# Optimization experiments

Hardware: AMD Instinct MI355X
Metric: run time of the kernel (lower is better)

The kernel has to match this reference:

```python
import jax, jax.numpy as jnp
from jax import lax
import numpy as np

B, C, T, S = 128, 512, 512, 128
L = 2 * S + 1  # blank-extended label length


def _ext_labels(seq, blank):
    # Channel index for each extended-label position s: blank at even s, seq[(s-1)//2] at odd s.
    s = jnp.arange(L)
    l = jnp.maximum(0, (s - 1) // 2)
    return jnp.where(s % 2 == 0, blank, seq[l])


def _alpha_pass(probs, lab):
    # probs: [C, T] per-frame probabilities; lab: [L] extended label channel ids.
    # Faithful to compute_alpha(): per-frame renormalization (Rabiner scaling) and
    # start-window masking (s >= L - 2*(T - t)); entries beyond end = 2t+2 are
    # structurally exact zeros, so summing the full masked column equals the
    # original's windowed sum.
    s = jnp.arange(L)
    p_ext = probs[lab, :].T  # [T, L]
    lab_m2 = jnp.concatenate([jnp.full((2,), -1, lab.dtype), lab[:-2]])
    # s-2 transition allowed only at odd s with non-repeated label (s==1 handled by zero pad).
    mask2 = (s % 2 == 1) & (lab != lab_m2)

    a0 = jnp.zeros(L, probs.dtype).at[0].set(p_ext[0, 0]).at[1].set(p_ext[0, 1])
    c0 = a0.sum()
    a0 = jnp.where(c0 > 0, a0 / c0, a0)

    def step(a_prev, inp):
        t, p_t = inp
        start = jnp.maximum(0, L - 2 * (T - t))
        a1 = jnp.concatenate([jnp.zeros(1, a_prev.dtype), a_prev[:-1]])
        a2 = jnp.concatenate([jnp.zeros(2, a_prev.dtype), a_prev[:-2]])
        a_new = (a_prev + a1 + jnp.where(mask2, a2, 0.0)) * p_t
        a_new = jnp.where(s >= start, a_new, 0.0)
        c = a_new.sum()
        a_new = jnp.where(c > 0, a_new / c, a_new)
        return a_new, a_new

    _, rest = lax.scan(step, a0, (jnp.arange(1, T), p_ext[1:]))
    return jnp.concatenate([a0[None, :], rest], axis=0).T  # [L, T]


def _ctc_single(probs, seq, blank):
    lab = _ext_labels(seq, blank)
    a = _alpha_pass(probs, lab)  # alphas
    # betas: alpha pass on time-reversed probs and reversed labels, then flip both axes
    lab_r = _ext_labels(jnp.flip(seq), blank)
    b = jnp.flip(_alpha_pass(jnp.flip(probs, axis=1), lab_r), axis=(0, 1))
    ab = a * b  # [L, T]
    p_ext = probs[lab, :]  # [L, T]
    lh = (ab / p_ext).sum(0)  # [T]
    return -jnp.sum(jnp.log(lh))


def setup_inputs() -> dict:
    key = jax.random.key(0)
    k1, k2 = jax.random.split(key)
    logits = jax.random.normal(k1, (B, C, T), dtype=jnp.float32)
    params = jax.nn.softmax(logits, axis=1)  # module consumes probabilities
    seq = jax.random.randint(k2, (B, S), 1, C, dtype=jnp.int32)  # labels never equal blank=0
    lengths = jnp.full((B,), 4 * T, dtype=jnp.int32)  # lengths//4 == T == params time dim
    return {"params": params, "seq": seq, "lengths": lengths, "blank": 0}


def reference(params, seq, lengths, blank):
    # lengths//4 == T (static, equals params.shape[2]) for all samples by construction.
    losses = jax.vmap(lambda p, q: _ctc_single(p, q, blank))(params, seq)
    return jnp.sum(losses)
```

## Files before the change

### kernel.cpp

```cpp
#include <hip/hip_runtime.h>
#include <math.h>


#define BB 128
#define CC 512
#define TT 512
#define SS 128
#define LL 257
#define LPADH 260

typedef unsigned int  uint;
typedef unsigned short ushort;

template<int CTRL>
__device__ __forceinline__ float dpp0_f32(float x){
    int v = __builtin_bit_cast(int, x);
    int r = __builtin_amdgcn_update_dpp(0, v, CTRL, 0xF, 0xF, true);
    return __builtin_bit_cast(float, r);
}
__device__ __forceinline__ float shfl_up1_f32(float x){ return dpp0_f32<0x138>(x); }
__device__ __forceinline__ float red8f(float x){
    x += dpp0_f32<0x111>(x);
    x += dpp0_f32<0x112>(x);
    x += dpp0_f32<0x114>(x);
    return x;
}
__device__ __forceinline__ float tail3f(float x){
    x += dpp0_f32<0x118>(x);
    x += dpp0_f32<0x142>(x);
    x += dpp0_f32<0x143>(x);
    return x;
}
__device__ __forceinline__ float full64f(float x){ return tail3f(red8f(x)); }
__device__ __forceinline__ float readlane63_f32(float x){
    int v = __builtin_bit_cast(int, x);
    return __builtin_bit_cast(float, __builtin_amdgcn_readlane(v, 63));
}
__device__ __forceinline__ float pow2if(int e){
    return __builtin_bit_cast(float, (127 + e) << 23);
}
__device__ __forceinline__ uint pk_bf16(float lo, float hi){
    return __builtin_amdgcn_perm(__builtin_bit_cast(uint, hi),
                                 __builtin_bit_cast(uint, lo), 0x07060302u);
}
__device__ __forceinline__ float up_lo(uint u){ return __builtin_bit_cast(float, u << 16); }
__device__ __forceinline__ float up_hi(uint u){ return __builtin_bit_cast(float, u & 0xFFFF0000u); }
__device__ __forceinline__ float up_us(ushort u){ return __builtin_bit_cast(float, ((uint)u) << 16); }
template<int CTRL>
__device__ __forceinline__ double dpp0_f64(double x){
    int2 v = __builtin_bit_cast(int2, x);
    int2 r;
    r.x = __builtin_amdgcn_update_dpp(0, v.x, CTRL, 0xF, 0xF, true);
    r.y = __builtin_amdgcn_update_dpp(0, v.y, CTRL, 0xF, 0xF, true);
    return __builtin_bit_cast(double, r);
}
__device__ __forceinline__ double full64d(double x){
    x += dpp0_f64<0x111>(x); x += dpp0_f64<0x112>(x); x += dpp0_f64<0x114>(x);
    x += dpp0_f64<0x118>(x); x += dpp0_f64<0x142>(x); x += dpp0_f64<0x143>(x);
    return x;
}

__device__ __forceinline__ void lds_barrier(){
    asm volatile("s_waitcnt lgkmcnt(0)" ::: "memory");
    __builtin_amdgcn_s_barrier();
    __builtin_amdgcn_sched_barrier(0);
    asm volatile("" ::: "memory");
}

template<bool REV>
__device__ __forceinline__ void scan_body(
    int b, int wv, int l, const float* __restrict__ P,
    const int* __restrict__ seqg, int blank,
    ushort* __restrict__ W, ushort* __restrict__ W4, int* __restrict__ Eb)
{
    __shared__ float4 st4[64];
    __shared__ float  st1[64];
    __shared__ float  scSh[1];

    const bool is63 = (l == 63);
    const float* Pb = P + (size_t)b * (CC*TT);
    const int* sq = seqg + b*SS;

    int r1, r3; float m1, m3;
    if (!REV) {
        r1 = sq[2*l]; r3 = sq[2*l+1];
        int ip = (l==0) ? 0 : (2*l-1);
        m1 = (l==0) ? 1.f : ((r1 != sq[ip]) ? 1.f : 0.f);
        m3 = (r3 != r1) ? 1.f : 0.f;
    } else {
        r1 = sq[SS-1-2*l]; r3 = sq[SS-2-2*l];
        int ip = (l==0) ? 0 : (SS-2*l);
        m1 = (l==0) ? 1.f : ((r1 != sq[ip]) ? 1.f : 0.f);
        m3 = (r3 != r1) ? 1.f : 0.f;
    }
    const float* pBp = Pb + (size_t)blank*TT;
    const float* p1p = Pb + (size_t)r1*TT;
    const float* p3p = Pb + (size_t)r3*TT;
    int* EbB = Eb + b*64;

    const int tm0=(4*l+769)>>1, tm1=(4*l+770)>>1, tm2=(4*l+771)>>1, tm3=(4*l+772)>>1;

    float a0=0.f,a1=0.f,a2=0.f,a3=0.f,a4=0.f;
    float scNext = 1.f, Sfull = 0.f;
    const float u0i = (l==0) ? 1.f : 0.f;
    float4 qB[4], q1[4], q3[4];
    uint sbLo[16], sbHi[16]; float s4f[16];

#define COMP4(v,c) ((c)==0?(v).x:((c)==1?(v).y:((c)==2?(v).z:(v).w)))

#define LOADPG2(ss)                                                         \
  { const int base_ = REV ? (TT - 16*(ss) - 4) : (16*(ss));                 \
    _Pragma("unroll")                                                       \
    for (int k=0;k<4;++k){                                                  \
      int c_ = REV ? (base_ - 4*k) : (base_ + 4*k);                         \
      qB[k] = *reinterpret_cast<const float4*>(pBp + c_);                   \
      q1[k] = *reinterpret_cast<const float4*>(p1p + c_);                   \
      q3[k] = *reinterpret_cast<const float4*>(p3p + c_);                   \
    } }

#define STEP16(ss, j, FIRSTF, MASKF)                                        \
  {                                                                         \
    const int i = 16*(ss) + (j);                                            \
    float u0,u1,u2,u3,u4;                                                   \
    if (FIRSTF) { u0=u0i; u1=u0i; u2=0.f; u3=0.f; u4=0.f; }                 \
    else {                                                                  \
      float e3u = shfl_up1_f32(a3);                                         \
      u0 = a0 + e3u; u1 = (a1+a0) + m1*e3u; u2 = a2+a1;                     \
      u3 = (a3+a2) + m3*a1; u4 = a4+a3;                                     \
      if (MASKF) {                                                          \
        if (i >= tm0) u0 = 0.f;                                             \
        if (i >= tm1) u1 = 0.f;                                             \
        if (i >= tm2) u2 = 0.f;                                             \
        if (i >= tm3) u3 = 0.f;                                             \
      }                                                                     \
    }                                                                       \
    constexpr int ch_ = (j) >> 2;                                           \
    constexpr int cm_ = REV ? ((3-(j)) & 3) : ((j) & 3);                    \
    float pB = COMP4(qB[ch_], cm_);                                         \
    float pq = COMP4(q1[ch_], cm_);                                         \
    float pr = COMP4(q3[ch_], cm_);                                         \
    if (((j)&7)==0) { pB*=scNext; pq*=scNext; pr*=scNext; }                 \
    float n0=u0*pB, n1=u1*pq, n2=u2*pB, n3=u3*pr, n4=u4*pB;                 \
    sbLo[j]=pk_bf16(n0,n1); sbHi[j]=pk_bf16(n2,n3); s4f[j]=n4;              \
    if (((j)&7)==5) {                                                       \
      float part=(n0+n1)+(n2+n3); if (is63) part+=n4;                       \
      Sfull = full64f(part);                                                \
    }                                                                       \
    if (((j)&7)==7) {                                                       \
      float Su = readlane63_f32(Sfull);                                     \
      int ex = (__builtin_bit_cast(int, Su) >> 23) & 0xFF;                  \
      int e = (ex==0) ? 0 : (ex-127);                                       \
      e = e < -120 ? -120 : (e > 120 ? 120 : e);                            \
      scNext = pow2if(-e);                                                  \
      const int g_ = i >> 3;                                                \
      if (REV && l==0 && g_+1 < 64) EbB[g_+1] = e;                          \
    }                                                                       \
    a0=n0; a1=n1; a2=n2; a3=n3; a4=n4;                                      \
  }

#define RG2(ss, FIRSTF, MASKF)                                              \
    STEP16(ss,0,FIRSTF,MASKF) STEP16(ss,1,false,MASKF)                      \
    STEP16(ss,2,false,MASKF)  STEP16(ss,3,false,MASKF)                      \
    STEP16(ss,4,false,MASKF)  STEP16(ss,5,false,MASKF)                      \
    STEP16(ss,6,false,MASKF)  STEP16(ss,7,false,MASKF)                      \
    STEP16(ss,8,false,MASKF)  STEP16(ss,9,false,MASKF)                      \
    STEP16(ss,10,false,MASKF) STEP16(ss,11,false,MASKF)                     \
    STEP16(ss,12,false,MASKF) STEP16(ss,13,false,MASKF)                     \
    STEP16(ss,14,false,MASKF) STEP16(ss,15,false,MASKF)

#define STOREROWS2(ss)                                                      \
  {                                                                         \
    ushort* Ww = W + ((size_t)b*TT + (size_t)(ss)*16) * LPADH;              \
    _Pragma("unroll")                                                       \
    for (int j=0;j<16;++j)                                                  \
      *reinterpret_cast<uint2*>(Ww + (size_t)j*LPADH + 4*l)                 \
          = make_uint2(sbLo[j], sbHi[j]);                                   \
    if (is63) {                                                             \
      uint4 pk0, pk1;                                                       \
      pk0.x = pk_bf16(s4f[0], s4f[1]);   pk0.y = pk_bf16(s4f[2], s4f[3]);   \
      pk0.z = pk_bf16(s4f[4], s4f[5]);   pk0.w = pk_bf16(s4f[6], s4f[7]);   \
      pk1.x = pk_bf16(s4f[8], s4f[9]);   pk1.y = pk_bf16(s4f[10], s4f[11]); \
      pk1.z = pk_bf16(s4f[12], s4f[13]); pk1.w = pk_bf16(s4f[14], s4f[15]); \
      ushort* w4p = W4 + (size_t)b*TT + (size_t)(ss)*16;                    \
      *reinterpret_cast<uint4*>(w4p)     = pk0;                             \
      *reinterpret_cast<uint4*>(w4p + 8) = pk1;                             \
    }                                                                       \
  }

    LOADPG2(wv)

    for (int s = 0; s < 32; ++s) {
        if ((s & 1) == wv) {
            if (s > 0) {
                float4 v = st4[l];
                a0 = v.x; a1 = v.y; a2 = v.z; a3 = v.w;
                a4 = st1[l];
                scNext = scSh[0];
            }
            if (s == 0)      { RG2(0, true,  false) }
            else if (s < 24) { RG2(s, false, false) }
            else             { RG2(s, false, true ) }
            st4[l] = make_float4(a0, a1, a2, a3);
            st1[l] = a4;
            if (l == 0) scSh[0] = scNext;
        } else {
            if (s >= 1) STOREROWS2(s-1)
            if (s >= 1 && s < 31) LOADPG2(s+1)
        }
        lds_barrier();
    }
    if (wv == 1) STOREROWS2(31)

#undef STEP16
#undef RG2
#undef STOREROWS2
#undef LOADPG2
#undef COMP4
}

__global__ __launch_bounds__(128, 1)
void ctc_scan(const float* __restrict__ P, const int* __restrict__ seqg,
              const int* __restrict__ blankp, ushort* __restrict__ Wa,
              ushort* __restrict__ Wb, ushort* __restrict__ W4a,
              ushort* __restrict__ W4b, int* __restrict__ Eb)
{
    const int bx = blockIdx.x;
    const int wv = threadIdx.x >> 6, l = threadIdx.x & 63;
    const int blank = blankp[0];
    if (bx < BB) scan_body<false>(bx,      wv, l, P, seqg, blank, Wa, W4a, Eb);
    else         scan_body<true >(bx - BB, wv, l, P, seqg, blank, Wb, W4b, Eb);
}

__global__ __launch_bounds__(64)
void ctc_combine(const ushort* __restrict__ Wa, const ushort* __restrict__ Wb,
                 const ushort* __restrict__ W4a, const ushort* __restrict__ W4b,
                 const int* __restrict__ Eb, const int* __restrict__ seqg,
                 double* __restrict__ Lq)
{
    const int b = blockIdx.x, q = blockIdx.y, l = threadIdx.x;
    const bool is63 = (l == 63);
    const int* sq = seqg + b*SS;
    const int r1 = sq[SS-1-2*l], r3 = sq[SS-2-2*l];
    const int ip = (l==0) ? 0 : (SS-2*l);
    const float m1 = (l==0) ? 1.f : ((r1 != sq[ip]) ? 1.f : 0.f);
    const float m3 = (r3 != r1) ? 1.f : 0.f;
    const int tm0=(4*l+769)>>1, tm1=(4*l+770)>>1, tm2=(4*l+771)>>1, tm3=(4*l+772)>>1;

    const ushort* WaB = Wa + (size_t)b*TT*LPADH;
    const ushort* WbB = Wb + (size_t)b*TT*LPADH;
    const ushort* W4aB = W4a + (size_t)b*TT;
    const ushort* W4bB = W4b + (size_t)b*TT;
    const int t0 = q*8;

    float Rcur;
    {
        const ushort* rw = WbB + (size_t)(TT-1-t0)*LPADH;
        uint2 xu = *reinterpret_cast<const uint2*>(rw + 4*l);
        float rnp = (up_lo(xu.x)+up_hi(xu.x))+(up_lo(xu.y)+up_hi(xu.y));
        if (is63) rnp += up_us(W4bB[TT-1-t0]);
        Rcur = full64f(rnp);
    }

    float PmN = 1.f, PmD = 1.f;
    int   Ei  = 0;

    #pragma unroll
    for (int k=0; k<8; ++k) {
        const int t = t0 + k;
        const int i = TT-1-t;
        const ushort* arow = WaB + (size_t)t*LPADH;
        uint2 au = *reinterpret_cast<const uint2*>(arow + (252 - 4*l));
        float av0 = up_lo(au.x), av1 = up_hi(au.x);
        float av2 = up_lo(au.y), av3 = up_hi(au.y);
        float a256 = up_us(W4aB[t]);
        float ar4 = shfl_up1_f32(av0);
        if (l == 0) ar4 = a256;

        float u0,u1,u2,u3,u4, rnext = 0.f;
        if (i > 0) {
            const ushort* rw = WbB + (size_t)(i-1)*LPADH;
            uint2 bu = *reinterpret_cast<const uint2*>(rw + 4*l);
            float bv0 = up_lo(bu.x), bv1 = up_hi(bu.x);
            float bv2 = up_lo(bu.y), bv3 = up_hi(bu.y);
            float b4 = up_us(W4bB[i-1]);
            float e3u = shfl_up1_f32(bv3);
            u0 = bv0 + e3u;
            u1 = (bv1 + bv0) + m1*e3u;
            u2 = bv2 + bv1;
            u3 = (bv3 + bv2) + m3*bv1;
            u4 = b4 + bv3;
            if (i >= TT - SS) {
                if (i >= tm0) u0 = 0.f;
                if (i >= tm1) u1 = 0.f;
                if (i >= tm2) u2 = 0.f;
                if (i >= tm3) u3 = 0.f;
            }
            rnext = (bv0+bv1)+(bv2+bv3);
            if (is63) rnext += b4;
        } else {
            u0 = (l==0)?1.f:0.f; u1 = u0; u2=0.f; u3=0.f; u4=0.f;
        }
        float trp = ar4*u0 + av3*u1 + av2*u2 + av1*u3;
        if (is63) trp += av0*u4;
        float sap = (av1 + av2) + (av3 + ar4);
        if (is63) sap += av0;

        float D  = full64f(trp);
        float S  = full64f(sap);
        float Rn = full64f(rnext);
        if (is63) {
            float dd = fmaxf(D, 1e-37f);
            uint bn = __builtin_bit_cast(uint, dd);
            Ei += (int)((bn >> 23) & 0xFFu) - 127;
            PmN *= __builtin_bit_cast(float, (bn & 0x807FFFFFu) | (127u<<23));
            float sr = fmaxf(S * Rcur, 1e-37f);
            uint bd = __builtin_bit_cast(uint, sr);
            Ei -= (int)((bd >> 23) & 0xFFu) - 127;
            PmD *= __builtin_bit_cast(float, (bd & 0x807FFFFFu) | (127u<<23));
            if (i > 0 && (i & 7) == 0) Ei -= Eb[b*64 + (i>>3)];
        }
        Rcur = Rn;
    }
    if (is63)
        Lq[b*64 + q] = log((double)PmN / (double)PmD) + (double)Ei * M_LN2;
}

__global__ __launch_bounds__(256)
void ctc_final(const double* __restrict__ Lq, float* __restrict__ out)
{
    const int t = threadIdx.x;
    double v = 0.0;
    #pragma unroll
    for (int k=0;k<32;++k) v += Lq[t + 256*k];
    double s = full64d(v);
    __shared__ double w[4];
    if ((t & 63) == 63) w[t>>6] = s;
    __syncthreads();
    if (t == 0) out[0] = (float)(-(w[0]+w[1]+w[2]+w[3]));
}

extern "C" void kernel_launch(void* const* d_in, const int* in_sizes, int n_in,
                              void* d_out, int out_size, void* d_ws, size_t ws_size,
                              hipStream_t stream)
{
    const float* P     = (const float*)d_in[0];
    const int*   seq   = (const int*)  d_in[1];
    const int*   blank = (const int*)  d_in[3];

    ushort* Wa  = (ushort*)d_ws;
    ushort* Wb  = Wa  + (size_t)BB*TT*LPADH;
    ushort* W4a = Wb  + (size_t)BB*TT*LPADH;
    ushort* W4b = W4a + (size_t)BB*TT;
    double* Lq  = (double*)(W4b + (size_t)BB*TT);
    int*    Eb  = (int*)(Lq + (size_t)BB*64);
    (void)ws_size; (void)in_sizes; (void)n_in; (void)out_size;

    ctc_scan<<<2*BB, 128, 0, stream>>>(P, seq, blank, Wa, Wb, W4a, W4b, Eb);
    ctc_combine<<<dim3(BB, 64), 64, 0, stream>>>(Wa, Wb, W4a, W4b, Eb, seq, Lq);
    ctc_final<<<1, 256, 0, stream>>>(Lq, (float*)d_out);
}
```

Measured before the change: 58.37 us.

## Pre-transpose gathered label probabilities into time-major layout before scan

Adds a transpose kernel that gathers the 128 label rows plus the blank row per batch into a time-major buffer [B,T,132]. The scan then reads one contiguous row per time step instead of three strided per-lane rows from the full [C,T] tensor. This is meant to make the scan's global loads coalesced across lanes, and the prefetch is moved ahead of the row stores. The cost is an extra kernel launch and an extra round trip of about 34 MB through memory for the transposed buffer.

After: 69.45 us. 19.0% more time.

```diff
diff --git a/kernel.cpp b/kernel.cpp
--- a/kernel.cpp
+++ b/kernel.cpp
@@ -8,6 +8,7 @@
 #define SS 128
 #define LL 257
 #define LPADH 260
+#define PXW 132
 
 typedef unsigned int  uint;
 typedef unsigned short ushort;
@@ -67,10 +68,44 @@
     asm volatile("" ::: "memory");
 }
 
+__global__ __launch_bounds__(256)
+void ctc_xpose(const float* __restrict__ P, const int* __restrict__ seqg,
+               const int* __restrict__ blankp, float* __restrict__ Px)
+{
+    __shared__ float tile[129][65];
+    const int b = blockIdx.x, t0 = blockIdx.y * 64;
+    const int tid = threadIdx.x;
+    const int blank = blankp[0];
+    const int* sq = seqg + b*SS;
+    const float* Pb = P + (size_t)b*(CC*TT);
+
+    #pragma unroll
+    for (int k0 = 0; k0 < 144; k0 += 16) {
+        int k = k0 + (tid >> 4);
+        if (k < 129) {
+            int row = (k < 128) ? sq[k] : blank;
+            int tl = (tid & 15) << 2;
+            float4 v = *reinterpret_cast<const float4*>(
+                           Pb + (size_t)row*TT + t0 + tl);
+            tile[k][tl]   = v.x; tile[k][tl+1] = v.y;
+            tile[k][tl+2] = v.z; tile[k][tl+3] = v.w;
+        }
+    }
+    __syncthreads();
+    #pragma unroll
+    for (int pass = 0; pass < 32; ++pass) {
+        int tl = (pass << 1) + (tid >> 7);
+        int k  = tid & 127;
+        float* dst = Px + ((size_t)b*TT + t0 + tl) * PXW;
+        dst[k] = tile[k][tl];
+        if (k == 0) dst[128] = tile[128][tl];
+    }
+}
+
 template<bool REV>
 __device__ __forceinline__ void scan_body(
-    int b, int wv, int l, const float* __restrict__ P,
-    const int* __restrict__ seqg, int blank,
+    int b, int wv, int l, const float* __restrict__ Px,
+    const int* __restrict__ seqg,
     ushort* __restrict__ W, ushort* __restrict__ W4, int* __restrict__ Eb)
 {
     __shared__ float4 st4[64];
@@ -78,24 +113,22 @@
     __shared__ float  scSh[1];
 
     const bool is63 = (l == 63);
-    const float* Pb = P + (size_t)b * (CC*TT);
     const int* sq = seqg + b*SS;
 
-    int r1, r3; float m1, m3;
+    float m1, m3;
     if (!REV) {
-        r1 = sq[2*l]; r3 = sq[2*l+1];
+        int r1 = sq[2*l], r3 = sq[2*l+1];
         int ip = (l==0) ? 0 : (2*l-1);
         m1 = (l==0) ? 1.f : ((r1 != sq[ip]) ? 1.f : 0.f);
         m3 = (r3 != r1) ? 1.f : 0.f;
     } else {
-        r1 = sq[SS-1-2*l]; r3 = sq[SS-2-2*l];
+        int r1 = sq[SS-1-2*l], r3 = sq[SS-2-2*l];
         int ip = (l==0) ? 0 : (SS-2*l);
         m1 = (l==0) ? 1.f : ((r1 != sq[ip]) ? 1.f : 0.f);
         m3 = (r3 != r1) ? 1.f : 0.f;
     }
-    const float* pBp = Pb + (size_t)blank*TT;
-    const float* p1p = Pb + (size_t)r1*TT;
-    const float* p3p = Pb + (size_t)r3*TT;
+    const float* PxB = Px + (size_t)b*TT*PXW;
+    const int koff = REV ? (126 - 2*l) : (2*l);
     int* EbB = Eb + b*64;
 
     const int tm0=(4*l+769)>>1, tm1=(4*l+770)>>1, tm2=(4*l+771)>>1, tm3=(4*l+772)>>1;
@@ -103,19 +136,17 @@
     float a0=0.f,a1=0.f,a2=0.f,a3=0.f,a4=0.f;
     float scNext = 1.f, Sfull = 0.f;
     const float u0i = (l==0) ? 1.f : 0.f;
-    float4 qB[4], q1[4], q3[4];
+    float2 q12[16]; float qb[16];
     uint sbLo[16], sbHi[16]; float s4f[16];
 
-#define COMP4(v,c) ((c)==0?(v).x:((c)==1?(v).y:((c)==2?(v).z:(v).w)))
-
-#define LOADPG2(ss)                                                         \
-  { const int base_ = REV ? (TT - 16*(ss) - 4) : (16*(ss));                 \
-    _Pragma("unroll")                                                       \
-    for (int k=0;k<4;++k){                                                  \
-      int c_ = REV ? (base_ - 4*k) : (base_ + 4*k);                         \
-      qB[k] = *reinterpret_cast<const float4*>(pBp + c_);                   \
-      q1[k] = *reinterpret_cast<const float4*>(p1p + c_);                   \
-      q3[k] = *reinterpret_cast<const float4*>(p3p + c_);                   \
+#define LOADPX(ss)                                                          \
+  { _Pragma("unroll")                                                       \
+    for (int j=0;j<16;++j){                                                 \
+      const int i_ = 16*(ss)+j;                                             \
+      const int t_ = REV ? (TT-1-i_) : i_;                                  \
+      const float* rowp_ = PxB + (size_t)t_*PXW;                            \
+      q12[j] = *reinterpret_cast<const float2*>(rowp_ + koff);              \
+      qb[j]  = rowp_[128];                                                  \
     } }
 
 #define STEP16(ss, j, FIRSTF, MASKF)                                        \
@@ -134,11 +165,9 @@
         if (i >= tm3) u3 = 0.f;                                             \
       }                                                                     \
     }                                                                       \
-    constexpr int ch_ = (j) >> 2;                                           \
-    constexpr int cm_ = REV ? ((3-(j)) & 3) : ((j) & 3);                    \
-    float pB = COMP4(qB[ch_], cm_);                                         \
-    float pq = COMP4(q1[ch_], cm_);                                         \
-    float pr = COMP4(q3[ch_], cm_);                                         \
+    float pB = qb[j];                                                       \
+    float pq = REV ? q12[j].y : q12[j].x;                                   \
+    float pr = REV ? q12[j].x : q12[j].y;                                   \
     if (((j)&7)==0) { pB*=scNext; pq*=scNext; pr*=scNext; }                 \
     float n0=u0*pB, n1=u1*pq, n2=u2*pB, n3=u3*pr, n4=u4*pB;                 \
     sbLo[j]=pk_bf16(n0,n1); sbHi[j]=pk_bf16(n2,n3); s4f[j]=n4;              \
@@ -187,7 +216,7 @@
     }                                                                       \
   }
 
-    LOADPG2(wv)
+    LOADPX(wv)
 
     for (int s = 0; s < 32; ++s) {
         if ((s & 1) == wv) {
@@ -204,8 +233,8 @@
             st1[l] = a4;
             if (l == 0) scSh[0] = scNext;
         } else {
+            if (s >= 1 && s < 31) LOADPX(s+1)
             if (s >= 1) STOREROWS2(s-1)
-            if (s >= 1 && s < 31) LOADPG2(s+1)
         }
         lds_barrier();
     }
@@ -214,21 +243,19 @@
 #undef STEP16
 #undef RG2
 #undef STOREROWS2
-#undef LOADPG2
-#undef COMP4
+#undef LOADPX
 }
 
 __global__ __launch_bounds__(128, 1)
-void ctc_scan(const float* __restrict__ P, const int* __restrict__ seqg,
-              const int* __restrict__ blankp, ushort* __restrict__ Wa,
-              ushort* __restrict__ Wb, ushort* __restrict__ W4a,
-              ushort* __restrict__ W4b, int* __restrict__ Eb)
+void ctc_scan(const float* __restrict__ Px, const int* __restrict__ seqg,
+              ushort* __restrict__ Wa, ushort* __restrict__ Wb,
+              ushort* __restrict__ W4a, ushort* __restrict__ W4b,
+              int* __restrict__ Eb)
 {
     const int bx = blockIdx.x;
     const int wv = threadIdx.x >> 6, l = threadIdx.x & 63;
-    const int blank = blankp[0];
-    if (bx < BB) scan_body<false>(bx,      wv, l, P, seqg, blank, Wa, W4a, Eb);
-    else         scan_body<true >(bx - BB, wv, l, P, seqg, blank, Wb, W4b, Eb);
+    if (bx < BB) scan_body<false>(bx,      wv, l, Px, seqg, Wa, W4a, Eb);
+    else         scan_body<true >(bx - BB, wv, l, Px, seqg, Wb, W4b, Eb);
 }
 
 __global__ __launch_bounds__(64)
@@ -353,9 +380,11 @@
     ushort* W4b = W4a + (size_t)BB*TT;
     double* Lq  = (double*)(W4b + (size_t)BB*TT);
     int*    Eb  = (int*)(Lq + (size_t)BB*64);
+    float*  Px  = (float*)(Eb + (size_t)BB*64);
     (void)ws_size; (void)in_sizes; (void)n_in; (void)out_size;
 
-    ctc_scan<<<2*BB, 128, 0, stream>>>(P, seq, blank, Wa, Wb, W4a, W4b, Eb);
+    ctc_xpose<<<dim3(BB, 8), 256, 0, stream>>>(P, seq, blank, Px);
+    ctc_scan<<<2*BB, 128, 0, stream>>>(Px, seq, Wa, Wb, W4a, W4b, Eb);
     ctc_combine<<<dim3(BB, 64), 64, 0, stream>>>(Wa, Wb, W4a, W4b, Eb, seq, Lq);
     ctc_final<<<1, 256, 0, stream>>>(Lq, (float*)d_out);
 }
```
